# Optimization experiments

Hardware: AMD Instinct MI355X
Metric: run time of the kernel (lower is better)

Reference implementation:

```python
import jax, jax.numpy as jnp
import numpy as np

SCALE = 0.0625      # spatial_scale
OUT = 7             # out_size (== part_size)
C_OUT = 256         # output_dim (== input channels, group_size=1)
SPP = 4             # sample_per_part
TRANS_STD = 0.1
FC_DIM = 1024
B, H, W = 4, 128, 128
N_ROI = 2000
IMG = 2048.0        # H / SCALE


def _round_half(x):
    # CUDA round(): half away from zero (coords are non-negative here)
    return jnp.floor(x + 0.5)


def deform_roi_pool(data, rois, offset):
    """Faithful port of deform_roi_pooling (DCNv2 deform PS-ROI pooling, group_size=1).
    data: [B,C,H,W]; rois: [N,5]; offset: None or [N,2,OUT,OUT]. Returns [N,C,OUT,OUT]."""
    Bn, C, Hh, Ww = data.shape
    N = rois.shape[0]
    b = rois[:, 0].astype(jnp.int32)
    sw = _round_half(rois[:, 1]) * SCALE - 0.5
    sh = _round_half(rois[:, 2]) * SCALE - 0.5
    ew = (_round_half(rois[:, 3]) + 1.0) * SCALE - 0.5
    eh = (_round_half(rois[:, 4]) + 1.0) * SCALE - 0.5
    rw = jnp.maximum(ew - sw, 0.1)
    rh = jnp.maximum(eh - sh, 0.1)
    bw, bh = rw / OUT, rh / OUT              # bin sizes
    subw, subh = bw / SPP, bh / SPP          # sub-bin sizes

    ph, pw = jnp.meshgrid(jnp.arange(OUT, dtype=data.dtype),
                          jnp.arange(OUT, dtype=data.dtype), indexing='ij')
    wstart = pw[None] * bw[:, None, None] + sw[:, None, None]   # [N,OUT,OUT]
    hstart = ph[None] * bh[:, None, None] + sh[:, None, None]
    if offset is not None:
        # part_size == out_size -> part index == bin index
        wstart = wstart + offset[:, 0] * TRANS_STD * rw[:, None, None]
        hstart = hstart + offset[:, 1] * TRANS_STD * rh[:, None, None]

    ih2, iw2 = jnp.meshgrid(jnp.arange(SPP, dtype=data.dtype),
                            jnp.arange(SPP, dtype=data.dtype), indexing='ij')
    ih2, iw2 = ih2.reshape(-1), iw2.reshape(-1)  # [SPP*SPP]
    # sample coords [S2, N, OUT, OUT]
    ws = wstart[None] + iw2[:, None, None, None] * subw[None, :, None, None]
    hs = hstart[None] + ih2[:, None, None, None] * subh[None, :, None, None]

    bb = b[:, None, None]  # [N,1,1]

    def body(carry, coords):
        acc, cnt = carry
        w, h = coords                                 # [N,OUT,OUT]
        valid = (w >= -0.5) & (w <= Ww - 0.5) & (h >= -0.5) & (h <= Hh - 0.5)
        wc = jnp.clip(w, 0.0, Ww - 1.0)
        hc = jnp.clip(h, 0.0, Hh - 1.0)
        x0 = jnp.floor(wc).astype(jnp.int32)
        y0 = jnp.floor(hc).astype(jnp.int32)
        x1 = jnp.minimum(x0 + 1, Ww - 1)
        y1 = jnp.minimum(y0 + 1, Hh - 1)
        dx = wc - x0
        dy = hc - y0
        v00 = data[bb, :, y0, x0]   # [N,OUT,OUT,C]
        v01 = data[bb, :, y0, x1]
        v10 = data[bb, :, y1, x0]
        v11 = data[bb, :, y1, x1]
        val = (((1 - dx) * (1 - dy))[..., None] * v00
               + (dx * (1 - dy))[..., None] * v01
               + ((1 - dx) * dy)[..., None] * v10
               + (dx * dy)[..., None] * v11)
        val = jnp.where(valid[..., None], val, 0.0)
        return (acc + val, cnt + valid.astype(data.dtype)), None

    init = (jnp.zeros((N, OUT, OUT, C), data.dtype),
            jnp.zeros((N, OUT, OUT), data.dtype))
    (s, cnt), _ = jax.lax.scan(body, init, (ws, hs))
    out = jnp.where(cnt[..., None] > 0, s / jnp.maximum(cnt, 1.0)[..., None], 0.0)
    return jnp.transpose(out, (0, 3, 1, 2))  # [N,C,OUT,OUT]


def setup_inputs() -> dict:
    key = jax.random.key(0)
    ks = jax.random.split(key, 16)
    data = jax.random.normal(ks[0], (B, C_OUT, H, W), dtype=jnp.float32)
    bidx = jax.random.randint(ks[1], (N_ROI,), 0, B).astype(jnp.float32)
    x1 = jax.random.uniform(ks[2], (N_ROI,), minval=0.0, maxval=IMG - 64.0)
    y1 = jax.random.uniform(ks[3], (N_ROI,), minval=0.0, maxval=IMG - 64.0)
    wbox = jax.random.uniform(ks[4], (N_ROI,), minval=16.0, maxval=400.0)
    hbox = jax.random.uniform(ks[5], (N_ROI,), minval=16.0, maxval=400.0)
    rois = jnp.stack([bidx, x1, y1,
                      jnp.minimum(x1 + wbox, IMG - 1.0),
                      jnp.minimum(y1 + hbox, IMG - 1.0)], axis=1)
    fin = OUT * OUT * C_OUT  # 12544
    def lin(k, i, o, s=None):
        s = (1.0 / np.sqrt(i)) if s is None else s
        return jax.random.normal(k, (i, o), dtype=jnp.float32) * s
    return {
        'data': data, 'rois': rois,
        'w1': lin(ks[6], fin, FC_DIM), 'b1': jnp.zeros((FC_DIM,), jnp.float32),
        'w2': lin(ks[7], FC_DIM, FC_DIM), 'b2': jnp.zeros((FC_DIM,), jnp.float32),
        'w3': lin(ks[8], FC_DIM, OUT * OUT * 2, 0.01), 'b3': jnp.zeros((OUT * OUT * 2,), jnp.float32),
        'mw1': lin(ks[9], fin, FC_DIM), 'mb1': jnp.zeros((FC_DIM,), jnp.float32),
        'mw2': lin(ks[10], FC_DIM, OUT * OUT, 0.01), 'mb2': jnp.zeros((OUT * OUT,), jnp.float32),
    }


def reference(data, rois, w1, b1, w2, b2, w3, b3, mw1, mb1, mw2, mb2):
    n = rois.shape[0]
    x = deform_roi_pool(data, rois, None)              # [N,C,OUT,OUT]
    xf = x.reshape(n, -1)
    h = jax.nn.relu(xf @ w1 + b1)
    h = jax.nn.relu(h @ w2 + b2)
    offset = (h @ w3 + b3).reshape(n, 2, OUT, OUT)
    m = jax.nn.relu(xf @ mw1 + mb1)
    mask = jax.nn.sigmoid(m @ mw2 + mb2).reshape(n, 1, OUT, OUT)
    feat = deform_roi_pool(data, rois, offset) * mask
    return feat
```

## Files before the change

### kernel.cpp

```cpp
#include <hip/hip_runtime.h>
#include <math.h>

#define WDIM 128
#define HDIM 128
#define BDIM 4
#define CDIM 256
#define NROI 2000
#define MPAD 2048
#define FIN  12544
#define FC   1024
#define HWC  (HDIM * WDIM * CDIM)

typedef unsigned short bf16r;
typedef unsigned short u16;
typedef __attribute__((ext_vector_type(8))) short bf16x8;
typedef __attribute__((ext_vector_type(4))) float f32x4;
typedef __attribute__((ext_vector_type(8))) _Float16 half8;
typedef __attribute__((ext_vector_type(8))) unsigned short ushort8v;

__device__ __forceinline__ bf16r f2bf(float f) {
    unsigned u = __float_as_uint(f);
    u += 0x7FFFu + ((u >> 16) & 1u);
    return (bf16r)(u >> 16);
}
__device__ __forceinline__ u16 f2h(float f) {
    union { u16 s; _Float16 h; } c; c.h = (_Float16)f; return c.s;
}

__device__ __forceinline__ void async16(const bf16r* g, bf16r* l) {
    __builtin_amdgcn_global_load_lds(
        (const __attribute__((address_space(1))) unsigned int*)g,
        (__attribute__((address_space(3))) unsigned int*)l, 16, 0, 0);
}

#define VMW(n) asm volatile("s_waitcnt vmcnt(" #n ")" ::: "memory")
#define BARRIER() __builtin_amdgcn_s_barrier()

__device__ __forceinline__ void roi_geom(const float* __restrict__ rois, int n,
                                         int& b, float& sw, float& sh,
                                         float& rw, float& rh) {
    const float* r = rois + (size_t)n * 5;
    b = (int)r[0];
    float r1 = floorf(r[1] + 0.5f);
    float r2 = floorf(r[2] + 0.5f);
    float r3 = floorf(r[3] + 0.5f);
    float r4 = floorf(r[4] + 0.5f);
    sw = r1 * 0.0625f - 0.5f;
    sh = r2 * 0.0625f - 0.5f;
    float ew = (r3 + 1.0f) * 0.0625f - 0.5f;
    float eh = (r4 + 1.0f) * 0.0625f - 0.5f;
    rw = fmaxf(ew - sw, 0.1f);
    rh = fmaxf(eh - sh, 0.1f);
}

__device__ __forceinline__ void build_geometry(
        int n, int tid, const float* __restrict__ rois,
        const float* __restrict__ offs,
        const float* __restrict__ maskb,
        float* axW, unsigned* axMeta, uint2* wpix, int* npx, float* scale) {
    if (tid < 98) {
        int po = tid >> 1, axis = tid & 1;
        int b; float sw, sh, rw, rh;
        roi_geom(rois, n, b, sw, sh, rw, rh);
        float bw = rw * (1.f / 7.f), bh = rh * (1.f / 7.f);
        int ph = po / 7, pw = po - ph * 7;
        float start, sub;
        if (axis == 0) {
            start = (float)pw * bw + sw;
            if (offs) start += offs[(size_t)n * 98 + po] * 0.1f * rw;
            sub = bw * 0.25f;
        } else {
            start = (float)ph * bh + sh;
            if (offs) start += offs[(size_t)n * 98 + 49 + po] * 0.1f * rh;
            sub = bh * 0.25f;
        }
        float wsl[5] = {0.f, 0.f, 0.f, 0.f, 0.f};
        int base = 0, cnt = 0, mx = 0, any = 0;
#pragma unroll
        for (int i = 0; i < 4; ++i) {
            float p = start + (float)i * sub;
            bool valid = (p >= -0.5f) & (p <= 127.5f);
            float pc = fminf(fmaxf(p, 0.f), 127.f);
            int p0 = (int)floorf(pc);
            float d = pc - (float)p0;
            int p1 = min(p0 + 1, 127);
            if (valid) {
                if (!any) { base = p0; any = 1; }
                int c0 = p0 - base, c1 = p1 - base;
                float w0 = 1.f - d;
#pragma unroll
                for (int k = 0; k < 5; ++k)
                    wsl[k] += ((c0 == k) ? w0 : 0.f) + ((c1 == k) ? d : 0.f);
                cnt++;
                mx = max(mx, c1);
            }
        }
        int N = any ? mx + 1 : 0;
        axMeta[tid] = (unsigned)(N | (cnt << 3) | (base << 6));
#pragma unroll
        for (int k = 0; k < 5; ++k) axW[tid * 5 + k] = wsl[k];
    }
    __syncthreads();
    if (tid < 245) {
        int po = tid / 5, r = tid - po * 5;
        unsigned mx_ = axMeta[po * 2], my_ = axMeta[po * 2 + 1];
        int NX = mx_ & 7, NY = my_ & 7;
        int bx = (mx_ >> 6) & 127, by = (my_ >> 6) & 127;
        if (r == 0) {
            int cntx = (mx_ >> 3) & 7, cnty = (my_ >> 3) & 7;
            int ct = cntx * cnty;
            float sc = (ct > 0) ? 1.f / (float)ct : 0.f;
            if (maskb) sc *= (ct > 0) ? maskb[(size_t)n * 49 + po] : 0.f;
            npx[po] = NX * NY;
            scale[po] = sc;
        }
        if (r < NY) {
            float wyr = axW[(po * 2 + 1) * 5 + r];
            unsigned rowoff = (unsigned)(((by + r) * 128 + bx) * 512);
#pragma unroll
            for (int c = 0; c < 5; ++c)
                if (c < NX)
                    wpix[po * 28 + r * NX + c] =
                        make_uint2(rowoff + (unsigned)c * 512u,
                                   __float_as_uint(wyr * axW[po * 2 * 5 + c]));
        }
    }
    __syncthreads();
}

__global__ __launch_bounds__(256) void transpose_kernel(const float* __restrict__ data,
                                                        u16* __restrict__ data_t) {
    __shared__ float t[32][33];
    int x0 = blockIdx.x << 5;
    int c0 = blockIdx.y << 5;
    int b  = blockIdx.z >> 7;
    int y  = blockIdx.z & 127;
    int tx = threadIdx.x, ty = threadIdx.y;
#pragma unroll
    for (int i = 0; i < 32; i += 8)
        t[ty + i][tx] = data[(((size_t)b * CDIM + c0 + ty + i) * HDIM + y) * WDIM + x0 + tx];
    __syncthreads();
#pragma unroll
    for (int i = 0; i < 32; i += 8)
        data_t[(((size_t)b * HDIM + y) * WDIM + x0 + ty + i) * CDIM + c0 + tx] = f2h(t[tx][ty + i]);
}

__global__ __launch_bounds__(256) void conv_kernel(const float* __restrict__ srcA,
                                                   const float* __restrict__ srcB,
                                                   int nsplit, int ncols, int Nout,
                                                   int K, int perm,
                                                   bf16r* __restrict__ dst) {
    __shared__ float t[32][33];
    int k0 = blockIdx.x << 5, n0 = blockIdx.y << 5;
    int tx = threadIdx.x & 31, ty = threadIdx.x >> 5;
#pragma unroll
    for (int i = 0; i < 32; i += 8) {
        int k = k0 + ty + i;
        int n = n0 + tx;
        const float* s = (n < nsplit) ? srcA : srcB;
        int col = (n < nsplit) ? n : n - nsplit;
        int row = perm ? ((k & 255) * 49 + (k >> 8)) : k;
        float v = (n < Nout && col < ncols) ? s[(size_t)row * ncols + col] : 0.f;
        t[ty + i][tx] = v;
    }
    __syncthreads();
#pragma unroll
    for (int i = 0; i < 32; i += 8) {
        int n = n0 + ty + i;
        if (n < Nout) dst[(size_t)n * K + k0 + tx] = f2bf(t[tx][ty + i]);
    }
}

__global__ __launch_bounds__(512) void pool1_kernel(const u16* __restrict__ data_t,
                                                    const float* __restrict__ rois,
                                                    bf16r* __restrict__ xf) {
    __shared__ float axW[98 * 5];
    __shared__ unsigned axMeta[98];
    __shared__ uint2 wpix[49 * 28];
    __shared__ int npx[49];
    __shared__ float scale[49];
    int n = blockIdx.x, tid = threadIdx.x;
    build_geometry(n, tid, rois, nullptr, nullptr, axW, axMeta, wpix, npx, scale);
    int b = (int)rois[(size_t)n * 5];
    int wave = tid >> 6, lane = tid & 63, shalf = lane >> 5, c8 = (lane & 31) << 3;
    const char* dpb = (const char*)(data_t + (size_t)b * HWC + c8);
    for (int po = wave * 2 + shalf; po < 49; po += 16) {
        int npe = npx[po];
        float sc = scale[po];
        const uint2* wp = wpix + po * 28;
        float a[8];
#pragma unroll
        for (int k = 0; k < 8; ++k) a[k] = 0.f;
        int p = 0;
        for (; p + 2 <= npe; p += 2) {
            uint2 q0 = wp[p], q1 = wp[p + 1];
            half8 v0 = *(const half8*)(dpb + q0.x);
            half8 v1 = *(const half8*)(dpb + q1.x);
            float w0 = __uint_as_float(q0.y), w1 = __uint_as_float(q1.y);
#pragma unroll
            for (int k = 0; k < 8; ++k) a[k] += w0 * (float)v0[k];
#pragma unroll
            for (int k = 0; k < 8; ++k) a[k] += w1 * (float)v1[k];
        }
        if (p < npe) {
            uint2 q0 = wp[p];
            half8 v0 = *(const half8*)(dpb + q0.x);
            float w0 = __uint_as_float(q0.y);
#pragma unroll
            for (int k = 0; k < 8; ++k) a[k] += w0 * (float)v0[k];
        }
        ushort8v o;
#pragma unroll
        for (int k = 0; k < 8; ++k) o[k] = f2bf(a[k] * sc);
        *(ushort8v*)(xf + (size_t)n * FIN + po * 256 + c8) = o;
    }
}

__global__ __launch_bounds__(512) void pool2_kernel(const u16* __restrict__ data_t,
                                                    const float* __restrict__ rois,
                                                    const float* __restrict__ offs,
                                                    const float* __restrict__ maskb,
                                                    float* __restrict__ out) {
    __shared__ float tile[49 * 128];
    __shared__ float axW[98 * 5];
    __shared__ unsigned axMeta[98];
    __shared__ uint2 wpix[49 * 28];
    __shared__ int npx[49];
    __shared__ float scale[49];
    int n = blockIdx.x, chalf = blockIdx.y, tid = threadIdx.x;
    build_geometry(n, tid, rois, offs, maskb, axW, axMeta, wpix, npx, scale);
    int b = (int)rois[(size_t)n * 5];
    int wave = tid >> 6, lane = tid & 63, q = lane >> 4, c8 = (lane & 15) << 3;
    const char* dpb = (const char*)(data_t + (size_t)b * HWC + chalf * 128 + c8);
    for (int po = wave * 4 + q; po < 49; po += 32) {
        int npe = npx[po];
        float sc = scale[po];
        const uint2* wp = wpix + po * 28;
        float a[8];
#pragma unroll
        for (int k = 0; k < 8; ++k) a[k] = 0.f;
        int p = 0;
        for (; p + 2 <= npe; p += 2) {
            uint2 q0 = wp[p], q1 = wp[p + 1];
            half8 v0 = *(const half8*)(dpb + q0.x);
            half8 v1 = *(const half8*)(dpb + q1.x);
            float w0 = __uint_as_float(q0.y), w1 = __uint_as_float(q1.y);
#pragma unroll
            for (int k = 0; k < 8; ++k) a[k] += w0 * (float)v0[k];
#pragma unroll
            for (int k = 0; k < 8; ++k) a[k] += w1 * (float)v1[k];
        }
        if (p < npe) {
            uint2 q0 = wp[p];
            half8 v0 = *(const half8*)(dpb + q0.x);
            float w0 = __uint_as_float(q0.y);
#pragma unroll
            for (int k = 0; k < 8; ++k) a[k] += w0 * (float)v0[k];
        }
        int cs = c8 ^ ((po & 7) << 3);
        float4 lo = make_float4(a[0] * sc, a[1] * sc, a[2] * sc, a[3] * sc);
        float4 hi = make_float4(a[4] * sc, a[5] * sc, a[6] * sc, a[7] * sc);
        *(float4*)&tile[po * 128 + cs] = lo;
        *(float4*)&tile[po * 128 + cs + 4] = hi;
    }
    __syncthreads();
    float* op = out + (size_t)n * FIN + (size_t)chalf * 6272;
    for (int i = tid; i < 6272; i += 512) {
        int c = i / 49, po = i - c * 49;
        op[i] = tile[po * 128 + (c ^ ((po & 7) << 3))];
    }
}

#define STAGE_A(buf, h, kt) do { \
    async16(Abase + (size_t)(kt) * 64 + sAoff[h][0], &lds[buf][0][((h) * 128 + wave * 8) * 64]); \
    async16(Abase + (size_t)(kt) * 64 + sAoff[h][1], &lds[buf][0][((h) * 128 + 64 + wave * 8) * 64]); \
} while (0)
#define STAGE_B(buf, h, kt) do { \
    async16(Bbase + (size_t)(kt) * 64 + sBoff[h][0], &lds[buf][1][((h) * 128 + wave * 8) * 64]); \
    async16(Bbase + (size_t)(kt) * 64 + sBoff[h][1], &lds[buf][1][((h) * 128 + 64 + wave * 8) * 64]); \
} while (0)
#define PHASE(buf, mh, nh, STAGE_STMT, GUARD_STMT) do { \
    const char* Ar = (const char*)&lds[buf][0][0] + aQ + (mh) * 16384; \
    const char* Br = (const char*)&lds[buf][1][0] + bQ + (nh) * 16384; \
    bf16x8 af[4][2], bfv[2][2]; \
    _Pragma("unroll") for (int i = 0; i < 4; ++i) \
        _Pragma("unroll") for (int ks = 0; ks < 2; ++ks) \
            af[i][ks] = *(const bf16x8*)(Ar + i * 2048 + fRB[ks]); \
    _Pragma("unroll") for (int jf = 0; jf < 2; ++jf) \
        _Pragma("unroll") for (int ks = 0; ks < 2; ++ks) \
            bfv[jf][ks] = *(const bf16x8*)(Br + jf * 2048 + fRB[ks]); \
    STAGE_STMT; \
    BARRIER(); \
    __builtin_amdgcn_s_setprio(1); \
    _Pragma("unroll") for (int i = 0; i < 4; ++i) \
        _Pragma("unroll") for (int jf = 0; jf < 2; ++jf) \
            _Pragma("unroll") for (int ks = 0; ks < 2; ++ks) \
                acc[(mh) * 4 + i][(nh) * 2 + jf] = __builtin_amdgcn_mfma_f32_16x16x32_bf16( \
                    af[i][ks], bfv[jf][ks], acc[(mh) * 4 + i][(nh) * 2 + jf], 0, 0, 0); \
    __builtin_amdgcn_s_setprio(0); \
    GUARD_STMT; \
    BARRIER(); \
} while (0)

__global__ __launch_bounds__(512, 2) void gemm256_kernel(
        const bf16r* __restrict__ A, int lda,
        const bf16r* __restrict__ Bt, int ldb,
        float* __restrict__ P, int Npad, int KS, int ktiles) {
    __shared__ bf16r lds[2][2][256 * 64];
    int tid = threadIdx.x;
    int wave = tid >> 6, lane = tid & 63;
    int l15 = lane & 15, quad = lane >> 4;
    int wm = wave >> 2, wn = wave & 3;

    int idx = blockIdx.x + gridDim.x * blockIdx.y;
    int nid = (idx & 7) * ((gridDim.x * gridDim.y) >> 3) + (idx >> 3);
    int bx = nid % gridDim.x, by = nid / gridDim.x;
    int m0 = by << 8, n0 = bx << 8;
    int z = blockIdx.z;

    int sAoff[2][2], sBoff[2][2];
#pragma unroll
    for (int h = 0; h < 2; ++h)
#pragma unroll
        for (int j = 0; j < 2; ++j) {
            int slot = h * 128 + j * 64 + wave * 8 + (lane >> 3);
            int g = (lane & 7) ^ ((slot >> 1) & 7);
            int rowA = ((slot >> 6) & 1) * 128 + (slot >> 7) * 64 + (slot & 63);
            int colB = ((slot >> 5) & 3) * 64 + (slot >> 7) * 32 + (slot & 31);
            sAoff[h][j] = rowA * lda + g * 8;
            sBoff[h][j] = colB * ldb + g * 8;
        }
    const bf16r* Abase = A + (size_t)m0 * lda;
    const bf16r* Bbase = Bt + (size_t)n0 * ldb;

    int fRB[2];
#pragma unroll
    for (int ks = 0; ks < 2; ++ks)
        fRB[ks] = l15 * 128 + ((((ks << 2) + quad) ^ ((l15 >> 1) & 7)) << 4);
    int aQ = wm * 8192;
    int bQ = wn * 4096;

    f32x4 acc[8][4];
#pragma unroll
    for (int i = 0; i < 8; ++i)
#pragma unroll
        for (int j = 0; j < 4; ++j) acc[i][j] = (f32x4){0.f, 0.f, 0.f, 0.f};

    int tb = ((ktiles * z) / KS) & ~1;
    int te = (z == KS - 1) ? ktiles : ((ktiles * (z + 1)) / KS) & ~1;
    int nit = (te - tb) >> 1;

    STAGE_A(0, 0, tb); STAGE_B(0, 0, tb); STAGE_A(0, 1, tb); STAGE_B(0, 1, tb);
    STAGE_A(1, 0, tb + 1); STAGE_B(1, 0, tb + 1);
    VMW(4);
    BARRIER();

    for (int it = 0; it < nit; ++it) {
        int t1 = tb + 2 * it + 1, nx0 = t1 + 1, nx1 = t1 + 2;
        bool last = (it == nit - 1);
        PHASE(0, 0, 0, { STAGE_A(1, 1, t1); }, {});
        PHASE(0, 0, 1, { STAGE_B(1, 1, t1); }, {});
        PHASE(0, 1, 0, { if (!last) STAGE_A(0, 0, nx0); }, {});
        PHASE(0, 1, 1, { if (!last) STAGE_B(0, 0, nx0); },
              { if (last) { VMW(0); } else { VMW(4); } });
        PHASE(1, 0, 0, { if (!last) STAGE_A(0, 1, nx0); }, {});
        PHASE(1, 0, 1, { if (!last) STAGE_B(0, 1, nx0); }, {});
        PHASE(1, 1, 0, { if (!last) STAGE_A(1, 0, nx1); }, {});
        PHASE(1, 1, 1, { if (!last) STAGE_B(1, 0, nx1); },
              { if (!last) { VMW(4); } });
    }

    float* Pp = P + (size_t)z * MPAD * Npad;
#pragma unroll
    for (int I = 0; I < 8; ++I) {
        int row = m0 + wm * 128 + I * 16 + quad * 4;
#pragma unroll
        for (int J = 0; J < 4; ++J) {
            int col = n0 + wn * 64 + J * 16 + l15;
            float* o = Pp + (size_t)row * Npad + col;
#pragma unroll
            for (int r = 0; r < 4; ++r) o[(size_t)r * Npad] = acc[I][J][r];
        }
    }
}

__global__ __launch_bounds__(256) void gemm_mfma_kernel(
        const bf16r* __restrict__ A, int lda,
        const bf16r* __restrict__ Bt, int K,
        float* __restrict__ P, int Npad, int KS) {
    __shared__ bf16r As[128 * 32];
    __shared__ bf16r Bs[128 * 32];
    int tid = threadIdx.x;
    int wave = tid >> 6, lane = tid & 63;
    int nwgxy = gridDim.x * gridDim.y;
    int idx = blockIdx.x + gridDim.x * blockIdx.y;
    int chunk = nwgxy >> 3;
    int nid = (idx & 7) * chunk + (idx >> 3);
    int bx = nid % gridDim.x, by = nid / gridDim.x;
    int m0 = by << 7, n0 = bx << 7;
    int z = blockIdx.z;

    int srow = lane >> 2;
    int kchunk = ((lane & 3) ^ ((lane >> 3) & 3)) << 3;
    const bf16r* aG0 = A + (size_t)(m0 + wave * 32 + srow) * lda + kchunk;
    const bf16r* aG1 = A + (size_t)(m0 + wave * 32 + 16 + srow) * lda + kchunk;
    const bf16r* bG0 = Bt + (size_t)(n0 + wave * 32 + srow) * K + kchunk;
    const bf16r* bG1 = Bt + (size_t)(n0 + wave * 32 + 16 + srow) * K + kchunk;
    bf16r* aL0 = As + wave * 1024;
    bf16r* aL1 = As + wave * 1024 + 512;
    bf16r* bL0 = Bs + wave * 1024;
    bf16r* bL1 = Bs + wave * 1024 + 512;

    int l15 = lane & 15, quad = lane >> 4;
    int wr = wave >> 1, wc = wave & 1;
    int psw = (quad ^ ((l15 >> 1) & 3)) << 3;
    int aoff[4], boff[4];
#pragma unroll
    for (int t = 0; t < 4; ++t) {
        aoff[t] = ((wr * 64 + t * 16 + l15) * 32 + psw) * 2;
        boff[t] = ((wc * 64 + t * 16 + l15) * 32 + psw) * 2;
    }

    f32x4 acc[4][4];
#pragma unroll
    for (int i = 0; i < 4; ++i)
#pragma unroll
        for (int j = 0; j < 4; ++j) acc[i][j] = (f32x4){0.f, 0.f, 0.f, 0.f};

    int iters = K >> 5;
    int i0 = (int)((long)iters * z / KS);
    int i1 = (int)((long)iters * (z + 1) / KS);

    {
        size_t k0 = (size_t)i0 << 5;
        async16(aG0 + k0, aL0); async16(aG1 + k0, aL1);
        async16(bG0 + k0, bL0); async16(bG1 + k0, bL1);
    }
    for (int it = i0; it < i1; ++it) {
        __syncthreads();
        bf16x8 af[4], bfv[4];
#pragma unroll
        for (int t = 0; t < 4; ++t) af[t] = *(const bf16x8*)((const char*)As + aoff[t]);
#pragma unroll
        for (int t = 0; t < 4; ++t) bfv[t] = *(const bf16x8*)((const char*)Bs + boff[t]);
        __syncthreads();
        if (it + 1 < i1) {
            size_t k0 = (size_t)(it + 1) << 5;
            async16(aG0 + k0, aL0); async16(aG1 + k0, aL1);
            async16(bG0 + k0, bL0); async16(bG1 + k0, bL1);
        }
#pragma unroll
        for (int i = 0; i < 4; ++i)
#pragma unroll
            for (int j = 0; j < 4; ++j)
                acc[i][j] = __builtin_amdgcn_mfma_f32_16x16x32_bf16(af[i], bfv[j], acc[i][j], 0, 0, 0);
    }

    float* Pp = P + (size_t)z * MPAD * Npad;
#pragma unroll
    for (int i = 0; i < 4; ++i) {
        int row = m0 + wr * 64 + i * 16 + quad * 4;
#pragma unroll
        for (int j = 0; j < 4; ++j) {
            int col = n0 + wc * 64 + j * 16 + l15;
            float* o = Pp + (size_t)row * Npad + col;
#pragma unroll
            for (int r = 0; r < 4; ++r) o[(size_t)r * Npad] = acc[i][j][r];
        }
    }
}

__global__ __launch_bounds__(256) void reduce_kernel(
        const float* __restrict__ P, int shift, int KS,
        const float* __restrict__ bias0, const float* __restrict__ bias1, int bsplit,
        void* __restrict__ Out, int ldo, int M, int Nreal, int outmode) {
    int idx = blockIdx.x * 256 + threadIdx.x;
    int Npad = 1 << shift;
    int row = idx >> shift, col = idx & (Npad - 1);
    float s = 0.f;
    size_t plane = (size_t)MPAD << shift;
    for (int zz = 0; zz < KS; ++zz) s += P[(size_t)zz * plane + idx];
    if (row < M && col < Nreal) {
        float b = (col < bsplit) ? bias0[col] : bias1[col - bsplit];
        float v = s + b;
        if (outmode == 0) {
            v = fmaxf(v, 0.f);
            ((bf16r*)Out)[(size_t)row * ldo + col] = f2bf(v);
        } else {
            if (outmode == 2) v = 1.f / (1.f + expf(-v));
            ((float*)Out)[(size_t)row * ldo + col] = v;
        }
    }
}

extern "C" void kernel_launch(void* const* d_in, const int* in_sizes, int n_in,
                              void* d_out, int out_size, void* d_ws, size_t ws_size,
                              hipStream_t stream) {
    const float* data = (const float*)d_in[0];
    const float* rois = (const float*)d_in[1];
    const float* w1   = (const float*)d_in[2];
    const float* b1   = (const float*)d_in[3];
    const float* w2   = (const float*)d_in[4];
    const float* b2   = (const float*)d_in[5];
    const float* w3   = (const float*)d_in[6];
    const float* b3   = (const float*)d_in[7];
    const float* mw1  = (const float*)d_in[8];
    const float* mb1  = (const float*)d_in[9];
    const float* mw2  = (const float*)d_in[10];
    const float* mb2  = (const float*)d_in[11];
    float* out = (float*)d_out;

    char* w = (char*)d_ws;
    size_t off = 0;
    auto carve = [&](size_t bytes) {
        void* p = w + off;
        off += (bytes + 255) & ~(size_t)255;
        return p;
    };
    u16* data_t   = (u16*)carve((size_t)BDIM * HDIM * WDIM * CDIM * 2);
    bf16r* xf     = (bf16r*)carve((size_t)MPAD * FIN * 2);
    bf16r* bt1    = (bf16r*)carve((size_t)MPAD * FIN * 2);
    bf16r* hm     = (bf16r*)carve((size_t)MPAD * 2048 * 2);
    bf16r* h2     = (bf16r*)carve((size_t)MPAD * 1024 * 2);
    bf16r* bt2    = (bf16r*)carve((size_t)1024 * 1024 * 2);
    bf16r* bt3    = (bf16r*)carve((size_t)128 * 1024 * 2);
    bf16r* bt4    = (bf16r*)carve((size_t)128 * 1024 * 2);
    float* offs   = (float*)carve((size_t)NROI * 98 * 4);
    float* maskb  = (float*)carve((size_t)NROI * 49 * 4);
    float* P      = (float*)(w + off);
    size_t plane  = (size_t)MPAD * 2048 * 4;
    size_t avail  = (ws_size > off) ? ws_size - off : 0;
    int use256 = (avail >= 4 * plane);

    conv_kernel<<<dim3(392, 64), 256, 0, stream>>>(w1, mw1, 1024, 1024, 2048, FIN, 1, bt1);
    conv_kernel<<<dim3(32, 32), 256, 0, stream>>>(w2, w2, 1 << 30, 1024, 1024, 1024, 0, bt2);
    conv_kernel<<<dim3(32, 4), 256, 0, stream>>>(w3, w3, 1 << 30, 98, 98, 1024, 0, bt3);
    conv_kernel<<<dim3(32, 2), 256, 0, stream>>>(mw2, mw2, 1 << 30, 49, 49, 1024, 0, bt4);
    transpose_kernel<<<dim3(4, 8, 512), dim3(32, 8), 0, stream>>>(data, data_t);
    pool1_kernel<<<dim3(NROI), 512, 0, stream>>>(data_t, rois, xf);

    if (use256) {
        gemm256_kernel<<<dim3(8, 8, 4), 512, 0, stream>>>(xf, FIN, bt1, FIN, P, 2048, 4, 196);
        reduce_kernel<<<16384, 256, 0, stream>>>(P, 11, 4, b1, mb1, 1024, hm, 2048, NROI, 2048, 0);
    } else {
        gemm_mfma_kernel<<<dim3(16, 16, 3), 256, 0, stream>>>(xf, FIN, bt1, FIN, P, 2048, 3);
        reduce_kernel<<<16384, 256, 0, stream>>>(P, 11, 3, b1, mb1, 1024, hm, 2048, NROI, 2048, 0);
    }
    gemm_mfma_kernel<<<dim3(8, 16, 4), 256, 0, stream>>>(hm, 2048, bt2, 1024, P, 1024, 4);
    reduce_kernel<<<8192, 256, 0, stream>>>(P, 10, 4, b2, b2, 1 << 30, h2, 1024, NROI, 1024, 0);
    gemm_mfma_kernel<<<dim3(1, 16, 8), 256, 0, stream>>>(h2, 1024, bt3, 1024, P, 128, 8);
    reduce_kernel<<<1024, 256, 0, stream>>>(P, 7, 8, b3, b3, 1 << 30, offs, 98, NROI, 98, 1);
    gemm_mfma_kernel<<<dim3(1, 16, 8), 256, 0, stream>>>(hm + 1024, 2048, bt4, 1024, P, 128, 8);
    reduce_kernel<<<1024, 256, 0, stream>>>(P, 7, 8, mb2, mb2, 1 << 30, maskb, 49, NROI, 49, 2);

    pool2_kernel<<<dim3(NROI, 2), 512, 0, stream>>>(data_t, rois, offs, maskb, out);
}
```

Measured before the change: 525.2 us.

## Reuse LDS fragments across GEMM phases and vectorize split-K reduce

The 256x256 GEMM main loop now orders its quadrant MMAs so that A or B fragments loaded from LDS are reused by the next quadrant (snake order 00,01,11,10). This cuts LDS fragment reads per tile roughly in half, at the cost of more live fragment registers. Separately, the split-K reduce kernel now processes four columns per thread with float4 loads, and its grid sizes are cut by four to match. The extra registers could reduce occupancy or cause spills in the 512-thread kernel.

```diff
diff --git a/kernel.cpp b/kernel.cpp
--- a/kernel.cpp
+++ b/kernel.cpp
@@ -279,27 +279,26 @@
     async16(Bbase + (size_t)(kt) * 64 + sBoff[h][0], &lds[buf][1][((h) * 128 + wave * 8) * 64]); \
     async16(Bbase + (size_t)(kt) * 64 + sBoff[h][1], &lds[buf][1][((h) * 128 + 64 + wave * 8) * 64]); \
 } while (0)
-#define PHASE(buf, mh, nh, STAGE_STMT, GUARD_STMT) do { \
+#define LDA_HALF(buf, mh) do { \
     const char* Ar = (const char*)&lds[buf][0][0] + aQ + (mh) * 16384; \
-    const char* Br = (const char*)&lds[buf][1][0] + bQ + (nh) * 16384; \
-    bf16x8 af[4][2], bfv[2][2]; \
     _Pragma("unroll") for (int i = 0; i < 4; ++i) \
         _Pragma("unroll") for (int ks = 0; ks < 2; ++ks) \
-            af[i][ks] = *(const bf16x8*)(Ar + i * 2048 + fRB[ks]); \
+            aF[i][ks] = *(const bf16x8*)(Ar + i * 2048 + fRB[ks]); \
+} while (0)
+#define LDB_HALF(dst, buf, nh) do { \
+    const char* Br = (const char*)&lds[buf][1][0] + bQ + (nh) * 16384; \
     _Pragma("unroll") for (int jf = 0; jf < 2; ++jf) \
         _Pragma("unroll") for (int ks = 0; ks < 2; ++ks) \
-            bfv[jf][ks] = *(const bf16x8*)(Br + jf * 2048 + fRB[ks]); \
-    STAGE_STMT; \
-    BARRIER(); \
+            dst[jf][ks] = *(const bf16x8*)(Br + jf * 2048 + fRB[ks]); \
+} while (0)
+#define MMA_Q(mh, nh, B) do { \
     __builtin_amdgcn_s_setprio(1); \
     _Pragma("unroll") for (int i = 0; i < 4; ++i) \
         _Pragma("unroll") for (int jf = 0; jf < 2; ++jf) \
             _Pragma("unroll") for (int ks = 0; ks < 2; ++ks) \
                 acc[(mh) * 4 + i][(nh) * 2 + jf] = __builtin_amdgcn_mfma_f32_16x16x32_bf16( \
-                    af[i][ks], bfv[jf][ks], acc[(mh) * 4 + i][(nh) * 2 + jf], 0, 0, 0); \
+                    aF[i][ks], B[jf][ks], acc[(mh) * 4 + i][(nh) * 2 + jf], 0, 0, 0); \
     __builtin_amdgcn_s_setprio(0); \
-    GUARD_STMT; \
-    BARRIER(); \
 } while (0)
 
 __global__ __launch_bounds__(512, 2) void gemm256_kernel(
@@ -345,6 +344,7 @@
     for (int i = 0; i < 8; ++i)
 #pragma unroll
         for (int j = 0; j < 4; ++j) acc[i][j] = (f32x4){0.f, 0.f, 0.f, 0.f};
+    bf16x8 aF[4][2], bF0[2][2], bF1[2][2];
 
     int tb = ((ktiles * z) / KS) & ~1;
     int te = (z == KS - 1) ? ktiles : ((ktiles * (z + 1)) / KS) & ~1;
@@ -358,16 +358,53 @@
     for (int it = 0; it < nit; ++it) {
         int t1 = tb + 2 * it + 1, nx0 = t1 + 1, nx1 = t1 + 2;
         bool last = (it == nit - 1);
-        PHASE(0, 0, 0, { STAGE_A(1, 1, t1); }, {});
-        PHASE(0, 0, 1, { STAGE_B(1, 1, t1); }, {});
-        PHASE(0, 1, 0, { if (!last) STAGE_A(0, 0, nx0); }, {});
-        PHASE(0, 1, 1, { if (!last) STAGE_B(0, 0, nx0); },
-              { if (last) { VMW(0); } else { VMW(4); } });
-        PHASE(1, 0, 0, { if (!last) STAGE_A(0, 1, nx0); }, {});
-        PHASE(1, 0, 1, { if (!last) STAGE_B(0, 1, nx0); }, {});
-        PHASE(1, 1, 0, { if (!last) STAGE_A(1, 0, nx1); }, {});
-        PHASE(1, 1, 1, { if (!last) STAGE_B(1, 0, nx1); },
-              { if (!last) { VMW(4); } });
+        LDA_HALF(0, 0); LDB_HALF(bF0, 0, 0);
+        STAGE_A(1, 1, t1);
+        BARRIER();
+        MMA_Q(0, 0, bF0);
+        BARRIER();
+
+        LDB_HALF(bF1, 0, 1);
+        STAGE_B(1, 1, t1);
+        BARRIER();
+        MMA_Q(0, 1, bF1);
+        BARRIER();
+
+        LDA_HALF(0, 1);
+        if (!last) STAGE_A(0, 0, nx0);
+        BARRIER();
+        MMA_Q(1, 1, bF1);
+        BARRIER();
+
+        if (!last) STAGE_B(0, 0, nx0);
+        BARRIER();
+        MMA_Q(1, 0, bF0);
+        if (last) { VMW(0); } else { VMW(4); }
+        BARRIER();
+
+        LDA_HALF(1, 0); LDB_HALF(bF0, 1, 0);
+        if (!last) STAGE_A(0, 1, nx0);
+        BARRIER();
+        MMA_Q(0, 0, bF0);
+        BARRIER();
+
+        LDB_HALF(bF1, 1, 1);
+        if (!last) STAGE_B(0, 1, nx0);
+        BARRIER();
+        MMA_Q(0, 1, bF1);
+        BARRIER();
+
+        LDA_HALF(1, 1);
+        if (!last) STAGE_A(1, 0, nx1);
+        BARRIER();
+        MMA_Q(1, 1, bF1);
+        BARRIER();
+
+        if (!last) STAGE_B(1, 0, nx1);
+        BARRIER();
+        MMA_Q(1, 0, bF0);
+        if (!last) { VMW(4); }
+        BARRIER();
     }
 
     float* Pp = P + (size_t)z * MPAD * Npad;
@@ -474,21 +511,27 @@
         const float* __restrict__ P, int shift, int KS,
         const float* __restrict__ bias0, const float* __restrict__ bias1, int bsplit,
         void* __restrict__ Out, int ldo, int M, int Nreal, int outmode) {
-    int idx = blockIdx.x * 256 + threadIdx.x;
+    int idx = (blockIdx.x * 256 + threadIdx.x) << 2;
     int Npad = 1 << shift;
     int row = idx >> shift, col = idx & (Npad - 1);
-    float s = 0.f;
+    f32x4 s = (f32x4){0.f, 0.f, 0.f, 0.f};
     size_t plane = (size_t)MPAD << shift;
-    for (int zz = 0; zz < KS; ++zz) s += P[(size_t)zz * plane + idx];
-    if (row < M && col < Nreal) {
-        float b = (col < bsplit) ? bias0[col] : bias1[col - bsplit];
-        float v = s + b;
-        if (outmode == 0) {
-            v = fmaxf(v, 0.f);
-            ((bf16r*)Out)[(size_t)row * ldo + col] = f2bf(v);
-        } else {
-            if (outmode == 2) v = 1.f / (1.f + expf(-v));
-            ((float*)Out)[(size_t)row * ldo + col] = v;
+    for (int zz = 0; zz < KS; ++zz) s += *(const f32x4*)(P + (size_t)zz * plane + idx);
+    if (row < M) {
+#pragma unroll
+        for (int e = 0; e < 4; ++e) {
+            int c = col + e;
+            if (c < Nreal) {
+                float b = (c < bsplit) ? bias0[c] : bias1[c - bsplit];
+                float v = s[e] + b;
+                if (outmode == 0) {
+                    v = fmaxf(v, 0.f);
+                    ((bf16r*)Out)[(size_t)row * ldo + c] = f2bf(v);
+                } else {
+                    if (outmode == 2) v = 1.f / (1.f + expf(-v));
+                    ((float*)Out)[(size_t)row * ldo + c] = v;
+                }
+            }
         }
     }
 }
@@ -541,17 +584,17 @@
 
     if (use256) {
         gemm256_kernel<<<dim3(8, 8, 4), 512, 0, stream>>>(xf, FIN, bt1, FIN, P, 2048, 4, 196);
-        reduce_kernel<<<16384, 256, 0, stream>>>(P, 11, 4, b1, mb1, 1024, hm, 2048, NROI, 2048, 0);
+        reduce_kernel<<<4096, 256, 0, stream>>>(P, 11, 4, b1, mb1, 1024, hm, 2048, NROI, 2048, 0);
     } else {
         gemm_mfma_kernel<<<dim3(16, 16, 3), 256, 0, stream>>>(xf, FIN, bt1, FIN, P, 2048, 3);
-        reduce_kernel<<<16384, 256, 0, stream>>>(P, 11, 3, b1, mb1, 1024, hm, 2048, NROI, 2048, 0);
+        reduce_kernel<<<4096, 256, 0, stream>>>(P, 11, 3, b1, mb1, 1024, hm, 2048, NROI, 2048, 0);
     }
     gemm_mfma_kernel<<<dim3(8, 16, 4), 256, 0, stream>>>(hm, 2048, bt2, 1024, P, 1024, 4);
-    reduce_kernel<<<8192, 256, 0, stream>>>(P, 10, 4, b2, b2, 1 << 30, h2, 1024, NROI, 1024, 0);
+    reduce_kernel<<<2048, 256, 0, stream>>>(P, 10, 4, b2, b2, 1 << 30, h2, 1024, NROI, 1024, 0);
     gemm_mfma_kernel<<<dim3(1, 16, 8), 256, 0, stream>>>(h2, 1024, bt3, 1024, P, 128, 8);
-    reduce_kernel<<<1024, 256, 0, stream>>>(P, 7, 8, b3, b3, 1 << 30, offs, 98, NROI, 98, 1);
+    reduce_kernel<<<256, 256, 0, stream>>>(P, 7, 8, b3, b3, 1 << 30, offs, 98, NROI, 98, 1);
     gemm_mfma_kernel<<<dim3(1, 16, 8), 256, 0, stream>>>(hm + 1024, 2048, bt4, 1024, P, 128, 8);
-    reduce_kernel<<<1024, 256, 0, stream>>>(P, 7, 8, mb2, mb2, 1 << 30, maskb, 49, NROI, 49, 2);
+    reduce_kernel<<<256, 256, 0, stream>>>(P, 7, 8, mb2, mb2, 1 << 30, maskb, 49, NROI, 49, 2);
 
     pool2_kernel<<<dim3(NROI, 2), 512, 0, stream>>>(data_t, rois, offs, maskb, out);
 }
```

Result: faster. 510.7 us (-2.8%).
